# Kernel optimization log

Measured on AMD Instinct MI355X. Metric: run time of the kernel, lower is better.

Reference implementation:

```python
import jax, jax.numpy as jnp
import numpy as np

NL, D, H = 12, 768, 12   # layers, d_model, heads (Clinical-Longformer config)
DH = D // H
FF = 4 * D
VOCAB = 50265
MAXPOS = 4098
W = 256                   # one-sided sliding window (attention_window=512 -> 256 per side)
EPS = 1e-5

def layer_norm(x, g, b):
    m = jnp.mean(x, axis=-1, keepdims=True)
    v = jnp.mean(jnp.square(x - m), axis=-1, keepdims=True)
    return (x - m) * jax.lax.rsqrt(v + EPS) * g + b

def sliding_window_attention(q, k, v, key_mask):
    # q,k,v: [B,H,S,dh]; key_mask: [B,S] float (1=keep). S must be a multiple of W.
    # Chunked banded attention: query chunk c attends to key chunks c-1,c,c+1,
    # then an exact |i-j| <= W band mask is applied (HF Longformer local attention).
    B, Hh, S, dh = q.shape
    nc = S // W
    kp = jnp.pad(k, ((0, 0), (0, 0), (W, W), (0, 0))).reshape(B, Hh, nc + 2, W, dh)
    vp = jnp.pad(v, ((0, 0), (0, 0), (W, W), (0, 0))).reshape(B, Hh, nc + 2, W, dh)
    kc = jnp.concatenate([kp[:, :, :-2], kp[:, :, 1:-1], kp[:, :, 2:]], axis=3)  # [B,H,nc,3W,dh]
    vc = jnp.concatenate([vp[:, :, :-2], vp[:, :, 1:-1], vp[:, :, 2:]], axis=3)
    mp = jnp.pad(key_mask, ((0, 0), (W, W))).reshape(B, nc + 2, W)
    mc = jnp.concatenate([mp[:, :-2], mp[:, 1:-1], mp[:, 2:]], axis=2)            # [B,nc,3W]
    qc = q.reshape(B, Hh, nc, W, dh)
    scores = jnp.einsum('bhcqd,bhckd->bhcqk', qc, kc) * (1.0 / np.sqrt(dh))      # [B,H,nc,W,3W]
    qi = jnp.arange(W)[:, None]
    kj = jnp.arange(3 * W)[None, :]
    band = (kj >= qi) & (kj <= qi + 2 * W)        # exact |i-j| <= W band within the 3-chunk window
    valid = band[None, None, None] & (mc[:, None, :, None, :] > 0)
    attn = jax.nn.softmax(jnp.where(valid, scores, -1e9), axis=-1)
    return jnp.einsum('bhcqk,bhckd->bhcqd', attn, vc).reshape(B, Hh, S, dh)

def encoder(input_ids, attention_mask, word_emb, pos_emb, type_emb, emb_g, emb_b, layer_params):
    B, S = input_ids.shape
    mask = attention_mask.astype(jnp.float32)
    # RoBERTa-style position ids with padding_idx=1
    pos_ids = jnp.cumsum(attention_mask, axis=1) * attention_mask + 1
    h = word_emb[input_ids] + pos_emb[pos_ids] + type_emb[0]
    h = layer_norm(h, emb_g, emb_b)

    def step(h, p):
        Wq, bq, Wk, bk, Wv, bv, Wo, bo, g1, b1, W1, c1, W2, c2, g2, b2 = p
        q = (h @ Wq + bq).reshape(B, S, H, DH).transpose(0, 2, 1, 3)
        k = (h @ Wk + bk).reshape(B, S, H, DH).transpose(0, 2, 1, 3)
        v = (h @ Wv + bv).reshape(B, S, H, DH).transpose(0, 2, 1, 3)
        a = sliding_window_attention(q, k, v, mask)
        o = a.transpose(0, 2, 1, 3).reshape(B, S, D) @ Wo + bo
        h = layer_norm(h + o, g1, b1)
        f = jax.nn.gelu(h @ W1 + c1, approximate=False) @ W2 + c2
        h = layer_norm(h + f, g2, b2)
        return h, None

    h, _ = jax.lax.scan(step, h, layer_params)
    return h[:, 0, :]   # report_feat = last_hidden_state[:, 0, :]

def setup_inputs():
    key = jax.random.key(0)
    ks = iter(jax.random.split(key, 16))
    s = 0.02
    B, S = 1, 2048
    def w(shape):
        return s * jax.random.normal(next(ks), shape, jnp.float32)
    inp = {}
    inp['input_ids'] = jax.random.randint(next(ks), (B, S), 0, VOCAB, dtype=jnp.int32)
    inp['attention_mask'] = jnp.ones((B, S), dtype=jnp.int32)
    inp['word_emb'] = w((VOCAB, D))
    inp['pos_emb'] = w((MAXPOS, D))
    inp['type_emb'] = w((2, D))
    inp['emb_g'] = jnp.ones((D,), jnp.float32)
    inp['emb_b'] = jnp.zeros((D,), jnp.float32)
    inp['Wq'] = w((NL, D, D)); inp['bq'] = jnp.zeros((NL, D), jnp.float32)
    inp['Wk'] = w((NL, D, D)); inp['bk'] = jnp.zeros((NL, D), jnp.float32)
    inp['Wv'] = w((NL, D, D)); inp['bv'] = jnp.zeros((NL, D), jnp.float32)
    inp['Wo'] = w((NL, D, D)); inp['bo'] = jnp.zeros((NL, D), jnp.float32)
    inp['g1'] = jnp.ones((NL, D), jnp.float32); inp['b1'] = jnp.zeros((NL, D), jnp.float32)
    inp['W1'] = w((NL, D, FF)); inp['c1'] = jnp.zeros((NL, FF), jnp.float32)
    inp['W2'] = w((NL, FF, D)); inp['c2'] = jnp.zeros((NL, D), jnp.float32)
    inp['g2'] = jnp.ones((NL, D), jnp.float32); inp['b2'] = jnp.zeros((NL, D), jnp.float32)
    return inp

def reference(input_ids, attention_mask, word_emb, pos_emb, type_emb, emb_g, emb_b,
              Wq, bq, Wk, bk, Wv, bv, Wo, bo, g1, b1, W1, c1, W2, c2, g2, b2):
    lp = (Wq, bq, Wk, bk, Wv, bv, Wo, bo, g1, b1, W1, c1, W2, c2, g2, b2)
    return encoder(input_ids, attention_mask, word_emb, pos_emb, type_emb, emb_g, emb_b, lp)
```

## Files before the change

### kernel.cpp

```cpp
#include <hip/hip_runtime.h>
#include <hip/hip_bf16.h>
#include <cmath>

#define S_LEN 2048
#define DM 768
#define NH 12
#define DHEAD 64
#define FF_DIM 3072
#define NLAYERS 12
#define WIN 256

typedef __attribute__((ext_vector_type(4))) float f32x4;
typedef __attribute__((ext_vector_type(8))) short s16x8;
typedef __attribute__((ext_vector_type(4))) short s16x4;
typedef __attribute__((ext_vector_type(4))) float fragc;

#define OFF_QKVT 0L
#define OFF_WOT  1769472L
#define OFF_W1T  2359296L
#define OFF_W2T  4718592L
#define WSLAB    7077888L

__device__ __forceinline__ float bf2f(ushort u) {
  union { unsigned u; float f; } v; v.u = ((unsigned)u) << 16; return v.f;
}
__device__ __forceinline__ ushort f2bf(float f) {
  union { float f; unsigned u; } v; v.f = f;
  unsigned r = v.u + 0x7fffu + ((v.u >> 16) & 1u);
  return (ushort)(r >> 16);
}

typedef __attribute__((address_space(1))) const void GVp;
typedef __attribute__((address_space(3))) void LVp;
__device__ __forceinline__ void gload16(const void* g, void* l) {
  __builtin_amdgcn_global_load_lds((GVp*)g, (LVp*)l, 16, 0, 0);
}

template<int EPI, int BM, int BN, bool SPLIT>
__global__ __launch_bounds__(256) void gemm_t(
    const ushort* __restrict__ A0, int lda,
    const ushort* __restrict__ B0, int ldb,
    void* __restrict__ C0, void* __restrict__ C1, int ldc,
    const float* __restrict__ bias0,
    const float* __restrict__ res0,
    int Kdim)
{
  constexpr int MF = BM / 32;
  constexpr int NF = BN / 32;
  constexpr int MT = S_LEN / BM;
  __shared__ ushort As[2][BM * 64];
  __shared__ ushort Bs[2][BN * 64];

  const int tid  = threadIdx.x;
  const int lane = tid & 63;
  const int wave = tid >> 6;
  const int z    = SPLIT ? blockIdx.z : 0;
  const int koff = z * Kdim;

  const int nwg = gridDim.x;
  const int o   = blockIdx.x;
  const int id2 = (o & 7) * (nwg >> 3) + (o >> 3);
  const int mt  = id2 % MT;
  const int nt  = id2 / MT;

  const long aoff = (long)mt * BM * lda;
  const long boff = (long)nt * BN * ldb;
  const long coff = (long)mt * BM * ldc + (long)nt * BN;
  const float* bias = bias0 ? bias0 + nt * BN : nullptr;

  fragc acc[MF][NF] = {};
  const int l15 = lane & 15;
  const int g   = lane >> 4;
  const int rx  = l15 & 7;
  const int MR0 = (wave & 1) * (BM / 2);
  const int NC0 = (wave >> 1) * (BN / 2);
  const int srow = lane >> 3;
  const int scol = ((lane & 7) ^ srow) * 8;

  auto stage = [&](int buf, int k0) {
    #pragma unroll
    for (int j = 0; j < BM / 32; j++) {
      int c = wave * (BM / 32) + j;
      gload16(A0 + aoff + (long)(c * 8 + srow) * lda + k0 + scol,
              (char*)&As[buf][0] + c * 1024);
    }
    #pragma unroll
    for (int j = 0; j < BN / 32; j++) {
      int c = wave * (BN / 32) + j;
      gload16(B0 + boff + (long)(c * 8 + srow) * ldb + k0 + scol,
              (char*)&Bs[buf][0] + c * 1024);
    }
  };

  stage(0, koff);
  __syncthreads();
  int cur = 0;
  for (int k0 = koff; k0 < koff + Kdim; k0 += 64) {
    if (k0 + 64 < koff + Kdim) stage(cur ^ 1, k0 + 64);
    s16x8 afr[MF][2], bfr[NF][2];
    #pragma unroll
    for (int ks = 0; ks < 2; ks++) {
      #pragma unroll
      for (int mi = 0; mi < MF; mi++)
        afr[mi][ks] = *(const s16x8*)((const char*)&As[cur][0] +
                      (MR0 + mi * 16 + l15) * 128 + (((ks * 4 + g) ^ rx) << 4));
      #pragma unroll
      for (int ni = 0; ni < NF; ni++)
        bfr[ni][ks] = *(const s16x8*)((const char*)&Bs[cur][0] +
                      (NC0 + ni * 16 + l15) * 128 + (((ks * 4 + g) ^ rx) << 4));
    }
    __builtin_amdgcn_s_setprio(1);
    #pragma unroll
    for (int ks = 0; ks < 2; ks++)
      #pragma unroll
      for (int mi = 0; mi < MF; mi++)
        #pragma unroll
        for (int ni = 0; ni < NF; ni++)
          acc[mi][ni] = __builtin_amdgcn_mfma_f32_16x16x32_bf16(afr[mi][ks], bfr[ni][ks], acc[mi][ni], 0, 0, 0);
    __builtin_amdgcn_s_setprio(0);
    __syncthreads();
    cur ^= 1;
  }

  ushort* Cb  = (ushort*)C0;
  ushort* Cb1 = (ushort*)(z == 0 ? C0 : C1);
  const int rb = g * 4;
  #pragma unroll
  for (int mi = 0; mi < MF; mi++)
  #pragma unroll
  for (int ni = 0; ni < NF; ni++)
  #pragma unroll
  for (int r = 0; r < 4; r++) {
    int row = MR0 + mi * 16 + rb + r;
    int col = NC0 + ni * 16 + l15;
    long ci = coff + (long)row * ldc + col;
    float v = acc[mi][ni][r];
    if (EPI == 0) {
      if (bias) v += bias[col];
      Cb[ci] = f2bf(v);
    } else if (EPI == 2) {
      v += bias[col];
      v = 0.5f * v * (1.0f + erff(v * 0.70710678118654752f));
      Cb[ci] = f2bf(v);
    } else {
      if (z == 0) v += bias[col] + res0[ci];
      Cb1[ci] = f2bf(v);
    }
  }
}

__global__ __launch_bounds__(256) void attn_k(
    const ushort* __restrict__ qkvb,
    const ushort* __restrict__ vbT,
    const int*    __restrict__ am,
    ushort*       __restrict__ aob)
{
  __shared__ ushort Qs[64 * 64];
  __shared__ ushort Ks[2][128 * 64];
  __shared__ ushort Vs[64 * 128];
  __shared__ ushort Ps[4][16 * 128];
  __shared__ float  ambias[768];

  const int tid  = threadIdx.x;
  const int lane = tid & 63;
  const int w    = tid >> 6;
  const int l15  = lane & 15;
  const int g    = lane >> 4;
  const int o    = blockIdx.x;
  const int id2  = (o & 7) * 48 + (o >> 3);
  const int h    = id2 >> 5;
  const int q0   = (id2 & 31) * 64;
  const int korigin = (q0 >> 8) * 256 - WIN;
  const int q    = q0 + w * 16 + l15;

  auto stageK = [&](int buf, int kt) {
    int tok0 = korigin + kt * 128;
    #pragma unroll
    for (int j = 0; j < 4; j++) {
      int c = w * 4 + j;
      int stored = c * 1024 + lane * 16;
      int row = stored >> 7;
      int within = (stored & 127) ^ ((row & 7) << 4);
      int tok = tok0 + row;
      tok = tok < 0 ? 0 : (tok > S_LEN - 1 ? S_LEN - 1 : tok);
      gload16(qkvb + (size_t)tok * 2304 + DM + h * DHEAD + (within >> 1),
              (char*)&Ks[buf][0] + stored);
    }
  };
  auto stageV = [&](int kt) {
    int tok0 = korigin + kt * 128;
    #pragma unroll
    for (int j = 0; j < 4; j++) {
      int c = w * 4 + j;
      int stored = c * 1024 + lane * 16;
      int row = stored >> 8;
      int within = (stored & 255) ^ ((row & 7) << 4);
      int tok = tok0 + (within >> 1);
      tok = tok < 0 ? 0 : (tok > S_LEN - 8 ? S_LEN - 8 : tok);
      gload16(vbT + ((size_t)h * DHEAD + row) * S_LEN + tok,
              (char*)Vs + stored);
    }
  };

  #pragma unroll
  for (int j = 0; j < 2; j++) {
    int c = w * 2 + j;
    int stored = c * 1024 + lane * 16;
    int row = stored >> 7;
    int within = (stored & 127) ^ ((row & 7) << 4);
    gload16(qkvb + (size_t)(q0 + row) * 2304 + h * DHEAD + (within >> 1),
            (char*)Qs + stored);
  }
  for (int j = tid; j < 768; j += 256) {
    int tok = korigin + j;
    bool ok = (tok >= 0) && (tok < S_LEN) && (am[tok] != 0);
    ambias[j] = ok ? 0.0f : -1e30f;
  }

  const int lo = q0 - WIN < 0 ? 0 : q0 - WIN;
  const int hi = (q0 + 63 + WIN > S_LEN - 1) ? S_LEN - 1 : q0 + 63 + WIN;
  const int kt_start = (lo - korigin) >> 7;
  const int kt_end   = (hi - korigin) >> 7;

  stageK(0, kt_start);
  stageV(kt_start);
  __syncthreads();

  s16x8 qf[2];
  #pragma unroll
  for (int ks = 0; ks < 2; ks++)
    qf[ks] = *(const s16x8*)((const char*)Qs + (w * 16 + l15) * 128 +
                             ((g * 16 + ks * 64) ^ ((l15 & 7) << 4)));

  f32x4 ot[4] = {};
  float m = -1e20f, l = 0.0f;
  int cur = 0;

  for (int kt = kt_start; kt <= kt_end; kt++) {
    if (kt < kt_end) stageK(cur ^ 1, kt + 1);

    f32x4 st[8] = {};
    __builtin_amdgcn_s_setprio(1);
    #pragma unroll
    for (int ks = 0; ks < 2; ks++) {
      #pragma unroll
      for (int mi = 0; mi < 8; mi++) {
        int row = mi * 16 + l15;
        s16x8 af = *(const s16x8*)((const char*)&Ks[cur][0] + row * 128 +
                                   ((g * 16 + ks * 64) ^ ((row & 7) << 4)));
        st[mi] = __builtin_amdgcn_mfma_f32_16x16x32_bf16(af, qf[ks], st[mi], 0, 0, 0);
      }
    }
    __builtin_amdgcn_s_setprio(0);

    float mx = -1e30f;
    float sv[8][4];
    #pragma unroll
    for (int mi = 0; mi < 8; mi++)
      #pragma unroll
      for (int r = 0; r < 4; r++) {
        int kw  = kt * 128 + mi * 16 + g * 4 + r;
        int tok = korigin + kw;
        float s = st[mi][r] * 0.125f + ambias[kw];
        bool band = (tok >= q - WIN) && (tok <= q + WIN);
        s = band ? s : -1e30f;
        sv[mi][r] = s;
        mx = fmaxf(mx, s);
      }
    mx = fmaxf(mx, __shfl_xor(mx, 16));
    mx = fmaxf(mx, __shfl_xor(mx, 32));

    float m_new = fmaxf(fmaxf(m, mx), -1e20f);
    float sf = __expf(m - m_new);
    float rs = 0.0f;
    #pragma unroll
    for (int mi = 0; mi < 8; mi++) {
      s16x4 pk;
      #pragma unroll
      for (int r = 0; r < 4; r++) {
        float p = __expf(sv[mi][r] - m_new);
        rs += p;
        pk[r] = (short)f2bf(p);
      }
      *(s16x4*)((char*)&Ps[w][0] + l15 * 256 + ((mi * 32 + g * 8) ^ ((l15 & 7) << 4))) = pk;
    }
    rs += __shfl_xor(rs, 16);
    rs += __shfl_xor(rs, 32);
    l = l * sf + rs;
    m = m_new;
    #pragma unroll
    for (int mi = 0; mi < 4; mi++)
      #pragma unroll
      for (int r = 0; r < 4; r++) ot[mi][r] *= sf;

    __syncthreads();

    __builtin_amdgcn_s_setprio(1);
    #pragma unroll
    for (int ks = 0; ks < 4; ks++) {
      s16x8 pf = *(const s16x8*)((const char*)&Ps[w][0] + l15 * 256 +
                                 ((ks * 64 + g * 16) ^ ((l15 & 7) << 4)));
      #pragma unroll
      for (int mi = 0; mi < 4; mi++) {
        int row = mi * 16 + l15;
        s16x8 vf = *(const s16x8*)((const char*)Vs + row * 256 +
                                   ((ks * 64 + g * 16) ^ ((row & 7) << 4)));
        ot[mi] = __builtin_amdgcn_mfma_f32_16x16x32_bf16(vf, pf, ot[mi], 0, 0, 0);
      }
    }
    __builtin_amdgcn_s_setprio(0);
    __syncthreads();

    if (kt < kt_end) stageV(kt + 1);
    cur ^= 1;
  }

  float inv = l > 0.0f ? 1.0f / l : 0.0f;
  #pragma unroll
  for (int mi = 0; mi < 4; mi++) {
    s16x4 oo;
    #pragma unroll
    for (int r = 0; r < 4; r++) oo[r] = (short)f2bf(ot[mi][r] * inv);
    *(s16x4*)(aob + (size_t)q * DM + h * DHEAD + mi * 16 + g * 4) = oo;
  }
}

__global__ __launch_bounds__(256) void cvtT_k(const float* __restrict__ src, ushort* __restrict__ dst,
                                              int N, int K, long sstride, long dstride, int dnoff)
{
  __shared__ float tile[32][33];
  const int tid = threadIdx.x;
  src += (long)blockIdx.z * sstride;
  dst += (long)blockIdx.z * dstride;
  int n0 = blockIdx.x * 32, k0 = blockIdx.y * 32;
  #pragma unroll
  for (int j = 0; j < 4; j++) {
    int r = j * 8 + (tid >> 5);
    int c = tid & 31;
    tile[r][c] = src[(long)(k0 + r) * N + n0 + c];
  }
  __syncthreads();
  #pragma unroll
  for (int j = 0; j < 4; j++) {
    int n = j * 8 + (tid >> 5);
    int k = tid & 31;
    dst[(long)(dnoff + n0 + n) * K + k0 + k] = f2bf(tile[k][n]);
  }
}

__global__ __launch_bounds__(256) void transv_k(const ushort* __restrict__ qkvb, ushort* __restrict__ vbT)
{
  __shared__ ushort tile[64][72];
  const int tid = threadIdx.x;
  const int h = blockIdx.y;
  const int t0 = blockIdx.x * 64;
  #pragma unroll
  for (int it = 0; it < 4; it++) {
    int r = it * 16 + (tid >> 4);
    int c = (tid & 15) * 4;
    *(s16x4*)&tile[r][c] = *(const s16x4*)&qkvb[(long)(t0 + r) * 2304 + 2 * DM + h * DHEAD + c];
  }
  __syncthreads();
  #pragma unroll
  for (int it = 0; it < 4; it++) {
    int d = it * 16 + (tid >> 4);
    int t = (tid & 15) * 4;
    s16x4 v;
    #pragma unroll
    for (int j = 0; j < 4; j++) v[j] = (short)tile[t + j][d];
    *(s16x4*)&vbT[((long)h * DHEAD + d) * S_LEN + t0 + t] = v;
  }
}

__global__ void biascat_k(const float* __restrict__ bq, const float* __restrict__ bk,
                          const float* __restrict__ bv, float* __restrict__ out)
{
  int i = blockIdx.x * 256 + threadIdx.x;
  if (i >= NLAYERS * 3 * DM) return;
  int l = i / (3 * DM), j = i % (3 * DM);
  const float* src = j < DM ? bq : (j < 2 * DM ? bk : bv);
  out[(long)l * 3 * DM + j] = src[(long)l * DM + (j % DM)];
}

__global__ __launch_bounds__(256) void ln2_k(const float* __restrict__ X, float* __restrict__ Y,
                                             ushort* __restrict__ Yb,
                                             const float* __restrict__ g, const float* __restrict__ b)
{
  int row  = (int)((blockIdx.x * blockDim.x + threadIdx.x) >> 6);
  int lane = threadIdx.x & 63;
  const float* x = X + (long)row * DM + lane * 12;
  float v[12]; float sum = 0.f;
  #pragma unroll
  for (int j = 0; j < 3; j++) {
    f32x4 t = *(const f32x4*)(x + j * 4);
    #pragma unroll
    for (int r = 0; r < 4; r++) { v[j * 4 + r] = t[r]; sum += t[r]; }
  }
  #pragma unroll
  for (int off = 32; off; off >>= 1) sum += __shfl_xor(sum, off);
  float mean = sum * (1.0f / 768.0f);
  float var = 0.f;
  #pragma unroll
  for (int i = 0; i < 12; i++) { float d = v[i] - mean; var += d * d; }
  #pragma unroll
  for (int off = 32; off; off >>= 1) var += __shfl_xor(var, off);
  float rstd = rsqrtf(var * (1.0f / 768.0f) + 1e-5f);
  float* y = Y + (long)row * DM + lane * 12;
  ushort* yb = Yb + (long)row * DM + lane * 12;
  const float* gg = g + lane * 12;
  const float* bb = b + lane * 12;
  #pragma unroll
  for (int j = 0; j < 3; j++) {
    f32x4 go = *(const f32x4*)(gg + j * 4);
    f32x4 bo = *(const f32x4*)(bb + j * 4);
    f32x4 yo; s16x4 yh;
    #pragma unroll
    for (int r = 0; r < 4; r++) {
      float t = (v[j * 4 + r] - mean) * rstd * go[r] + bo[r];
      yo[r] = t; yh[r] = (short)f2bf(t);
    }
    *(f32x4*)(y + j * 4) = yo;
    *(s16x4*)(yb + j * 4) = yh;
  }
}

__global__ __launch_bounds__(256) void ln2db_k(const ushort* __restrict__ X0, const ushort* __restrict__ X1,
                                               float* __restrict__ Y, ushort* __restrict__ Yb,
                                               const float* __restrict__ g, const float* __restrict__ b)
{
  int row  = (int)((blockIdx.x * blockDim.x + threadIdx.x) >> 6);
  int lane = threadIdx.x & 63;
  const ushort* x0 = X0 + (long)row * DM + lane * 12;
  const ushort* x1 = X1 + (long)row * DM + lane * 12;
  float v[12]; float sum = 0.f;
  #pragma unroll
  for (int j = 0; j < 3; j++) {
    s16x4 a = *(const s16x4*)(x0 + j * 4);
    s16x4 c = *(const s16x4*)(x1 + j * 4);
    #pragma unroll
    for (int r = 0; r < 4; r++) {
      float t = bf2f((ushort)a[r]) + bf2f((ushort)c[r]);
      v[j * 4 + r] = t; sum += t;
    }
  }
  #pragma unroll
  for (int off = 32; off; off >>= 1) sum += __shfl_xor(sum, off);
  float mean = sum * (1.0f / 768.0f);
  float var = 0.f;
  #pragma unroll
  for (int i = 0; i < 12; i++) { float d = v[i] - mean; var += d * d; }
  #pragma unroll
  for (int off = 32; off; off >>= 1) var += __shfl_xor(var, off);
  float rstd = rsqrtf(var * (1.0f / 768.0f) + 1e-5f);
  float* y = Y + (long)row * DM + lane * 12;
  ushort* yb = Yb + (long)row * DM + lane * 12;
  const float* gg = g + lane * 12;
  const float* bb = b + lane * 12;
  #pragma unroll
  for (int j = 0; j < 3; j++) {
    f32x4 go = *(const f32x4*)(gg + j * 4);
    f32x4 bo = *(const f32x4*)(bb + j * 4);
    f32x4 yo; s16x4 yh;
    #pragma unroll
    for (int r = 0; r < 4; r++) {
      float t = (v[j * 4 + r] - mean) * rstd * go[r] + bo[r];
      yo[r] = t; yh[r] = (short)f2bf(t);
    }
    *(f32x4*)(y + j * 4) = yo;
    *(s16x4*)(yb + j * 4) = yh;
  }
}

__global__ void scan_k(const int* __restrict__ am, int* __restrict__ pos)
{
  __shared__ int buf[S_LEN];
  int t = threadIdx.x;
  buf[t] = am[t]; buf[t + 1024] = am[t + 1024];
  __syncthreads();
  for (int off = 1; off < S_LEN; off <<= 1) {
    int a0 = buf[t];
    int a1 = buf[t + 1024];
    int b0 = (t >= off) ? buf[t - off] : 0;
    int b1 = (t + 1024 >= off) ? buf[t + 1024 - off] : 0;
    __syncthreads();
    buf[t] = a0 + b0; buf[t + 1024] = a1 + b1;
    __syncthreads();
  }
  pos[t]        = buf[t] * am[t] + 1;
  pos[t + 1024] = buf[t + 1024] * am[t + 1024] + 1;
}

__global__ __launch_bounds__(256) void embed_k(const int* __restrict__ ids, const int* __restrict__ pos,
    const float* __restrict__ we, const float* __restrict__ pe, const float* __restrict__ te,
    float* __restrict__ out)
{
  int s = blockIdx.x / 3;
  int d = (blockIdx.x % 3) * 256 + threadIdx.x;
  out[(long)s * DM + d] = we[(long)ids[s] * DM + d] + pe[(long)pos[s] * DM + d] + te[d];
}

__global__ void out_k(const float* __restrict__ h, float* __restrict__ out)
{
  int i = blockIdx.x * 256 + threadIdx.x;
  if (i < DM) out[i] = h[i];
}

extern "C" void kernel_launch(void* const* d_in, const int* in_sizes, int n_in,
                              void* d_out, int out_size, void* d_ws, size_t ws_size,
                              hipStream_t stream)
{
  const int*   ids = (const int*)d_in[0];
  const int*   am  = (const int*)d_in[1];
  const float* we  = (const float*)d_in[2];
  const float* pe  = (const float*)d_in[3];
  const float* te  = (const float*)d_in[4];
  const float* eg  = (const float*)d_in[5];
  const float* eb  = (const float*)d_in[6];
  const float* Wq  = (const float*)d_in[7];
  const float* bq  = (const float*)d_in[8];
  const float* Wk  = (const float*)d_in[9];
  const float* bk  = (const float*)d_in[10];
  const float* Wv  = (const float*)d_in[11];
  const float* bv  = (const float*)d_in[12];
  const float* Wo  = (const float*)d_in[13];
  const float* bo  = (const float*)d_in[14];
  const float* g1  = (const float*)d_in[15];
  const float* b1  = (const float*)d_in[16];
  const float* W1  = (const float*)d_in[17];
  const float* c1  = (const float*)d_in[18];
  const float* W2  = (const float*)d_in[19];
  const float* c2  = (const float*)d_in[20];
  const float* g2  = (const float*)d_in[21];
  const float* b2  = (const float*)d_in[22];

  char* w = (char*)d_ws;
  float*  h    = (float*)w;  w += (size_t)S_LEN * DM * 4;
  float*  tmp  = (float*)w;  w += (size_t)S_LEN * DM * 4;
  float*  tmp2 = (float*)w;  w += (size_t)S_LEN * DM * 4;
  ushort* hb   = (ushort*)w; w += (size_t)S_LEN * DM * 2;
  ushort* qkvb = (ushort*)w; w += (size_t)S_LEN * 3 * DM * 2;
  ushort* vbT  = (ushort*)w; w += (size_t)NH * DHEAD * S_LEN * 2;
  ushort* aob  = (ushort*)w; w += (size_t)S_LEN * DM * 2;
  ushort* ffnb = (ushort*)w; w += (size_t)S_LEN * FF_DIM * 2;
  ushort* wT   = (ushort*)w; w += (size_t)NLAYERS * WSLAB * 2;
  float*  bqkv = (float*)w;  w += (size_t)NLAYERS * 3 * DM * 4;
  int*    pos  = (int*)w;

  ushort* tb0 = (ushort*)tmp;
  ushort* tb1 = (ushort*)tmp2;

  scan_k<<<1, 1024, 0, stream>>>(am, pos);
  embed_k<<<dim3(S_LEN * 3), 256, 0, stream>>>(ids, pos, we, pe, te, tmp);
  ln2_k<<<dim3(S_LEN / 4), 256, 0, stream>>>(tmp, h, hb, eg, eb);
  biascat_k<<<dim3((NLAYERS * 3 * DM + 255) / 256), 256, 0, stream>>>(bq, bk, bv, bqkv);
  cvtT_k<<<dim3(24, 24, NLAYERS), 256, 0, stream>>>(Wq, wT + OFF_QKVT, DM, DM, (long)DM*DM, WSLAB, 0);
  cvtT_k<<<dim3(24, 24, NLAYERS), 256, 0, stream>>>(Wk, wT + OFF_QKVT, DM, DM, (long)DM*DM, WSLAB, DM);
  cvtT_k<<<dim3(24, 24, NLAYERS), 256, 0, stream>>>(Wv, wT + OFF_QKVT, DM, DM, (long)DM*DM, WSLAB, 2*DM);
  cvtT_k<<<dim3(24, 24, NLAYERS), 256, 0, stream>>>(Wo, wT + OFF_WOT, DM, DM, (long)DM*DM, WSLAB, 0);
  cvtT_k<<<dim3(96, 24, NLAYERS), 256, 0, stream>>>(W1, wT + OFF_W1T, FF_DIM, DM, (long)DM*FF_DIM, WSLAB, 0);
  cvtT_k<<<dim3(24, 96, NLAYERS), 256, 0, stream>>>(W2, wT + OFF_W2T, DM, FF_DIM, (long)DM*FF_DIM, WSLAB, 0);

  for (int L = 0; L < NLAYERS; L++) {
    const ushort* wTL = wT + (size_t)L * WSLAB;

    gemm_t<0,64,128,false><<<dim3(576), 256, 0, stream>>>(
        hb, DM, wTL + OFF_QKVT, DM, qkvb, nullptr, 3 * DM,
        bqkv + (size_t)L * 3 * DM, nullptr, DM);
    transv_k<<<dim3(S_LEN / 64, NH), 256, 0, stream>>>(qkvb, vbT);

    attn_k<<<dim3(384), 256, 0, stream>>>(qkvb, vbT, am, aob);

    gemm_t<3,64,64,true><<<dim3(384, 1, 2), 256, 0, stream>>>(
        aob, DM, wTL + OFF_WOT, DM, tb0, tb1, DM,
        bo + (size_t)L * DM, h, 384);
    ln2db_k<<<dim3(S_LEN / 4), 256, 0, stream>>>(tb0, tb1, h, hb,
        g1 + (size_t)L * DM, b1 + (size_t)L * DM);

    gemm_t<2,64,128,false><<<dim3(768), 256, 0, stream>>>(
        hb, DM, wTL + OFF_W1T, DM, ffnb, nullptr, FF_DIM,
        c1 + (size_t)L * FF_DIM, nullptr, DM);
    gemm_t<3,64,64,true><<<dim3(384, 1, 2), 256, 0, stream>>>(
        ffnb, FF_DIM, wTL + OFF_W2T, FF_DIM, tb0, tb1, DM,
        c2 + (size_t)L * DM, h, 1536);
    ln2db_k<<<dim3(S_LEN / 4), 256, 0, stream>>>(tb0, tb1, h, hb,
        g2 + (size_t)L * DM, b2 + (size_t)L * DM);
  }

  out_k<<<3, 256, 0, stream>>>(h, (float*)d_out);
}
```

Before: 1.486 ms.

## Fuse V transpose into QKV GEMM, merge weight conversions, use fp32 split-K partials

The QKV GEMM epilogue now writes the V columns directly in transposed layout, so the separate transpose kernel is no longer launched per layer. The six weight-conversion launches are merged into one kernel. Split-K partials for the Wo and W2 GEMMs are now stored as fp32 instead of bf16, and the layernorm reads fp32, which doubles partial traffic but avoids the extra bf16 rounding. The MFMA priority hints (s_setprio) are also removed. Together these trim launches and transpose traffic at the cost of more bytes in the split-K path.

Result: no change. 1.510 ms (+1.6%).

```diff
diff --git a/kernel.cpp b/kernel.cpp
--- a/kernel.cpp
+++ b/kernel.cpp
@@ -36,14 +36,15 @@
   __builtin_amdgcn_global_load_lds((GVp*)g, (LVp*)l, 16, 0, 0);
 }
 
-template<int EPI, int BM, int BN, bool SPLIT>
+template<int EPI, int BM, int BN, bool SPLIT, bool VOUT>
 __global__ __launch_bounds__(256) void gemm_t(
     const ushort* __restrict__ A0, int lda,
     const ushort* __restrict__ B0, int ldb,
     void* __restrict__ C0, void* __restrict__ C1, int ldc,
     const float* __restrict__ bias0,
     const float* __restrict__ res0,
-    int Kdim)
+    int Kdim,
+    ushort* __restrict__ vbTp)
 {
   constexpr int MF = BM / 32;
   constexpr int NF = BN / 32;
@@ -109,7 +110,6 @@
         bfr[ni][ks] = *(const s16x8*)((const char*)&Bs[cur][0] +
                       (NC0 + ni * 16 + l15) * 128 + (((ks * 4 + g) ^ rx) << 4));
     }
-    __builtin_amdgcn_s_setprio(1);
     #pragma unroll
     for (int ks = 0; ks < 2; ks++)
       #pragma unroll
@@ -117,34 +117,41 @@
         #pragma unroll
         for (int ni = 0; ni < NF; ni++)
           acc[mi][ni] = __builtin_amdgcn_mfma_f32_16x16x32_bf16(afr[mi][ks], bfr[ni][ks], acc[mi][ni], 0, 0, 0);
-    __builtin_amdgcn_s_setprio(0);
     __syncthreads();
     cur ^= 1;
   }
 
-  ushort* Cb  = (ushort*)C0;
-  ushort* Cb1 = (ushort*)(z == 0 ? C0 : C1);
+  ushort* Cb = (ushort*)C0;
+  float*  Cf = (float*)(z == 0 ? C0 : C1);
   const int rb = g * 4;
   #pragma unroll
   for (int mi = 0; mi < MF; mi++)
   #pragma unroll
-  for (int ni = 0; ni < NF; ni++)
-  #pragma unroll
-  for (int r = 0; r < 4; r++) {
-    int row = MR0 + mi * 16 + rb + r;
-    int col = NC0 + ni * 16 + l15;
-    long ci = coff + (long)row * ldc + col;
-    float v = acc[mi][ni][r];
-    if (EPI == 0) {
-      if (bias) v += bias[col];
-      Cb[ci] = f2bf(v);
-    } else if (EPI == 2) {
-      v += bias[col];
-      v = 0.5f * v * (1.0f + erff(v * 0.70710678118654752f));
-      Cb[ci] = f2bf(v);
+  for (int ni = 0; ni < NF; ni++) {
+    const int row0 = MR0 + mi * 16 + rb;
+    const int col  = NC0 + ni * 16 + l15;
+    if (EPI == 0 && VOUT && nt >= 12) {
+      s16x4 pk;
+      #pragma unroll
+      for (int r = 0; r < 4; r++) pk[r] = (short)f2bf(acc[mi][ni][r] + bias[col]);
+      *(s16x4*)(vbTp + (size_t)(nt * BN - 1536 + col) * S_LEN + mt * BM + row0) = pk;
     } else {
-      if (z == 0) v += bias[col] + res0[ci];
-      Cb1[ci] = f2bf(v);
+      #pragma unroll
+      for (int r = 0; r < 4; r++) {
+        long ci = coff + (long)(row0 + r) * ldc + col;
+        float v = acc[mi][ni][r];
+        if (EPI == 0) {
+          if (bias) v += bias[col];
+          Cb[ci] = f2bf(v);
+        } else if (EPI == 2) {
+          v += bias[col];
+          v = 0.5f * v * (1.0f + erff(v * 0.70710678118654752f));
+          Cb[ci] = f2bf(v);
+        } else {
+          if (z == 0) v += bias[col] + res0[ci];
+          Cf[ci] = v;
+        }
+      }
     }
   }
 }
@@ -325,14 +332,35 @@
   }
 }
 
-__global__ __launch_bounds__(256) void cvtT_k(const float* __restrict__ src, ushort* __restrict__ dst,
-                                              int N, int K, long sstride, long dstride, int dnoff)
+__global__ __launch_bounds__(256) void cvtall_k(
+    const float* __restrict__ Wq, const float* __restrict__ Wk,
+    const float* __restrict__ Wv, const float* __restrict__ Wo,
+    const float* __restrict__ W1, const float* __restrict__ W2,
+    ushort* __restrict__ wT)
 {
   __shared__ float tile[32][33];
   const int tid = threadIdx.x;
-  src += (long)blockIdx.z * sstride;
-  dst += (long)blockIdx.z * dstride;
-  int n0 = blockIdx.x * 32, k0 = blockIdx.y * 32;
+  const size_t L = blockIdx.y;
+  int t = blockIdx.x;
+  const float* src; ushort* dst; int N, K, nx, ky, dnoff = 0;
+  if (t < 2304) {
+    int region = t / 576, tt = t % 576;
+    N = DM; K = DM; nx = tt % 24; ky = tt / 24;
+    src = (region == 0 ? Wq : region == 1 ? Wk : region == 2 ? Wv : Wo) + L * DM * DM;
+    if (region < 3) { dst = wT + L * WSLAB + OFF_QKVT; dnoff = region * DM; }
+    else            { dst = wT + L * WSLAB + OFF_WOT; }
+  } else if (t < 4608) {
+    int tt = t - 2304;
+    N = FF_DIM; K = DM; nx = tt % 96; ky = tt / 96;
+    src = W1 + L * DM * FF_DIM;
+    dst = wT + L * WSLAB + OFF_W1T;
+  } else {
+    int tt = t - 4608;
+    N = DM; K = FF_DIM; nx = tt % 24; ky = tt / 24;
+    src = W2 + L * DM * FF_DIM;
+    dst = wT + L * WSLAB + OFF_W2T;
+  }
+  const int n0 = nx * 32, k0 = ky * 32;
   #pragma unroll
   for (int j = 0; j < 4; j++) {
     int r = j * 8 + (tid >> 5);
@@ -345,30 +373,6 @@
     int n = j * 8 + (tid >> 5);
     int k = tid & 31;
     dst[(long)(dnoff + n0 + n) * K + k0 + k] = f2bf(tile[k][n]);
-  }
-}
-
-__global__ __launch_bounds__(256) void transv_k(const ushort* __restrict__ qkvb, ushort* __restrict__ vbT)
-{
-  __shared__ ushort tile[64][72];
-  const int tid = threadIdx.x;
-  const int h = blockIdx.y;
-  const int t0 = blockIdx.x * 64;
-  #pragma unroll
-  for (int it = 0; it < 4; it++) {
-    int r = it * 16 + (tid >> 4);
-    int c = (tid & 15) * 4;
-    *(s16x4*)&tile[r][c] = *(const s16x4*)&qkvb[(long)(t0 + r) * 2304 + 2 * DM + h * DHEAD + c];
-  }
-  __syncthreads();
-  #pragma unroll
-  for (int it = 0; it < 4; it++) {
-    int d = it * 16 + (tid >> 4);
-    int t = (tid & 15) * 4;
-    s16x4 v;
-    #pragma unroll
-    for (int j = 0; j < 4; j++) v[j] = (short)tile[t + j][d];
-    *(s16x4*)&vbT[((long)h * DHEAD + d) * S_LEN + t0 + t] = v;
   }
 }
 
@@ -424,22 +428,22 @@
   }
 }
 
-__global__ __launch_bounds__(256) void ln2db_k(const ushort* __restrict__ X0, const ushort* __restrict__ X1,
-                                               float* __restrict__ Y, ushort* __restrict__ Yb,
-                                               const float* __restrict__ g, const float* __restrict__ b)
+__global__ __launch_bounds__(256) void ln2d_k(const float* __restrict__ X0, const float* __restrict__ X1,
+                                              float* __restrict__ Y, ushort* __restrict__ Yb,
+                                              const float* __restrict__ g, const float* __restrict__ b)
 {
   int row  = (int)((blockIdx.x * blockDim.x + threadIdx.x) >> 6);
   int lane = threadIdx.x & 63;
-  const ushort* x0 = X0 + (long)row * DM + lane * 12;
-  const ushort* x1 = X1 + (long)row * DM + lane * 12;
+  const float* x0 = X0 + (long)row * DM + lane * 12;
+  const float* x1 = X1 + (long)row * DM + lane * 12;
   float v[12]; float sum = 0.f;
   #pragma unroll
   for (int j = 0; j < 3; j++) {
-    s16x4 a = *(const s16x4*)(x0 + j * 4);
-    s16x4 c = *(const s16x4*)(x1 + j * 4);
+    f32x4 a = *(const f32x4*)(x0 + j * 4);
+    f32x4 c = *(const f32x4*)(x1 + j * 4);
     #pragma unroll
     for (int r = 0; r < 4; r++) {
-      float t = bf2f((ushort)a[r]) + bf2f((ushort)c[r]);
+      float t = a[r] + c[r];
       v[j * 4 + r] = t; sum += t;
     }
   }
@@ -546,43 +550,34 @@
   float*  bqkv = (float*)w;  w += (size_t)NLAYERS * 3 * DM * 4;
   int*    pos  = (int*)w;
 
-  ushort* tb0 = (ushort*)tmp;
-  ushort* tb1 = (ushort*)tmp2;
-
   scan_k<<<1, 1024, 0, stream>>>(am, pos);
   embed_k<<<dim3(S_LEN * 3), 256, 0, stream>>>(ids, pos, we, pe, te, tmp);
   ln2_k<<<dim3(S_LEN / 4), 256, 0, stream>>>(tmp, h, hb, eg, eb);
   biascat_k<<<dim3((NLAYERS * 3 * DM + 255) / 256), 256, 0, stream>>>(bq, bk, bv, bqkv);
-  cvtT_k<<<dim3(24, 24, NLAYERS), 256, 0, stream>>>(Wq, wT + OFF_QKVT, DM, DM, (long)DM*DM, WSLAB, 0);
-  cvtT_k<<<dim3(24, 24, NLAYERS), 256, 0, stream>>>(Wk, wT + OFF_QKVT, DM, DM, (long)DM*DM, WSLAB, DM);
-  cvtT_k<<<dim3(24, 24, NLAYERS), 256, 0, stream>>>(Wv, wT + OFF_QKVT, DM, DM, (long)DM*DM, WSLAB, 2*DM);
-  cvtT_k<<<dim3(24, 24, NLAYERS), 256, 0, stream>>>(Wo, wT + OFF_WOT, DM, DM, (long)DM*DM, WSLAB, 0);
-  cvtT_k<<<dim3(96, 24, NLAYERS), 256, 0, stream>>>(W1, wT + OFF_W1T, FF_DIM, DM, (long)DM*FF_DIM, WSLAB, 0);
-  cvtT_k<<<dim3(24, 96, NLAYERS), 256, 0, stream>>>(W2, wT + OFF_W2T, DM, FF_DIM, (long)DM*FF_DIM, WSLAB, 0);
+  cvtall_k<<<dim3(6912, NLAYERS), 256, 0, stream>>>(Wq, Wk, Wv, Wo, W1, W2, wT);
 
   for (int L = 0; L < NLAYERS; L++) {
     const ushort* wTL = wT + (size_t)L * WSLAB;
 
-    gemm_t<0,64,128,false><<<dim3(576), 256, 0, stream>>>(
+    gemm_t<0,64,128,false,true><<<dim3(576), 256, 0, stream>>>(
         hb, DM, wTL + OFF_QKVT, DM, qkvb, nullptr, 3 * DM,
-        bqkv + (size_t)L * 3 * DM, nullptr, DM);
-    transv_k<<<dim3(S_LEN / 64, NH), 256, 0, stream>>>(qkvb, vbT);
+        bqkv + (size_t)L * 3 * DM, nullptr, DM, vbT);
 
     attn_k<<<dim3(384), 256, 0, stream>>>(qkvb, vbT, am, aob);
 
-    gemm_t<3,64,64,true><<<dim3(384, 1, 2), 256, 0, stream>>>(
-        aob, DM, wTL + OFF_WOT, DM, tb0, tb1, DM,
-        bo + (size_t)L * DM, h, 384);
-    ln2db_k<<<dim3(S_LEN / 4), 256, 0, stream>>>(tb0, tb1, h, hb,
+    gemm_t<3,64,64,true,false><<<dim3(384, 1, 2), 256, 0, stream>>>(
+        aob, DM, wTL + OFF_WOT, DM, tmp, tmp2, DM,
+        bo + (size_t)L * DM, h, 384, nullptr);
+    ln2d_k<<<dim3(S_LEN / 4), 256, 0, stream>>>(tmp, tmp2, h, hb,
         g1 + (size_t)L * DM, b1 + (size_t)L * DM);
 
-    gemm_t<2,64,128,false><<<dim3(768), 256, 0, stream>>>(
+    gemm_t<2,64,128,false,false><<<dim3(768), 256, 0, stream>>>(
         hb, DM, wTL + OFF_W1T, DM, ffnb, nullptr, FF_DIM,
-        c1 + (size_t)L * FF_DIM, nullptr, DM);
-    gemm_t<3,64,64,true><<<dim3(384, 1, 2), 256, 0, stream>>>(
-        ffnb, FF_DIM, wTL + OFF_W2T, FF_DIM, tb0, tb1, DM,
-        c2 + (size_t)L * DM, h, 1536);
-    ln2db_k<<<dim3(S_LEN / 4), 256, 0, stream>>>(tb0, tb1, h, hb,
+        c1 + (size_t)L * FF_DIM, nullptr, DM, nullptr);
+    gemm_t<3,64,64,true,false><<<dim3(384, 1, 2), 256, 0, stream>>>(
+        ffnb, FF_DIM, wTL + OFF_W2T, FF_DIM, tmp, tmp2, DM,
+        c2 + (size_t)L * DM, h, 1536, nullptr);
+    ln2d_k<<<dim3(S_LEN / 4), 256, 0, stream>>>(tmp, tmp2, h, hb,
         g2 + (size_t)L * DM, b2 + (size_t)L * DM);
   }
 
```
